# Kernel tuning notes

Measured on AMD Instinct MI355X. Metric: run time of the kernel, lower is better.

The kernel has to match this reference:

```python
import jax, jax.numpy as jnp
import numpy as np

THRESHOLD = 0.5
EPS = 1e-6

def cxcywh_to_xyxy(b):
    return jnp.concatenate([b[..., :2] - b[..., 2:] / 2, b[..., :2] + b[..., 2:] / 2], axis=-1)

def xyxy_to_cxcywh(b):
    return jnp.concatenate([(b[..., :2] + b[..., 2:]) / 2, b[..., 2:] - b[..., :2]], axis=-1)

def iou_matrix(a, b, eps):
    # a: [P,4] xyxy, b: [O,4] xyxy -> [P,O]
    lb = jnp.maximum(a[:, None, :2], b[None, :, :2])
    ub = jnp.minimum(a[:, None, 2:], b[None, :, 2:])
    wh = jnp.clip(ub - lb, 0.0)
    inter = wh[..., 0] * wh[..., 1]
    area_a = (a[:, 2] - a[:, 0]) * (a[:, 3] - a[:, 1])
    area_b = (b[:, 2] - b[:, 0]) * (b[:, 3] - b[:, 1])
    union = area_a[:, None] + area_b[None, :] - inter
    return inter / (union + eps)

def match_single(priors_xyxy, t_xyxy, t_labels):
    # SSD-style matching (stand-in for Calculate_bbox_target_classes)
    n_obj = t_xyxy.shape[0]
    iou = iou_matrix(priors_xyxy, t_xyxy, EPS)          # [P,O]
    best_obj_iou = jnp.max(iou, axis=1)                 # [P]
    best_obj = jnp.argmax(iou, axis=1)                  # [P]
    best_prior = jnp.argmax(iou, axis=0)                # [O] force-match each object
    best_obj = best_obj.at[best_prior].set(jnp.arange(n_obj))
    best_obj_iou = best_obj_iou.at[best_prior].set(1.0)
    labels = t_labels[best_obj]                          # [P]
    labels = jnp.where(best_obj_iou < THRESHOLD, 0, labels)
    locs = xyxy_to_cxcywh(t_xyxy[best_obj])              # [P,4] cxcywh
    return labels, locs

def setup_inputs() -> dict:
    key = jax.random.key(0)
    k1, k2, k3, k4, k5, k6, k7 = jax.random.split(key, 7)
    B, P, C, O = 64, 8732, 81, 32
    # predictions: cxcywh-ish boxes in [0,1]
    pl_xy = jax.random.uniform(k1, (B, P, 2))
    pl_wh = jax.random.uniform(k2, (B, P, 2)) * 0.25 + 0.02
    predictlocs = jnp.concatenate([pl_xy, pl_wh], axis=-1)
    predictcls = jax.random.normal(k3, (B, P, C))
    pr_xy = jax.random.uniform(k4, (P, 2))
    pr_wh = jax.random.uniform(k5, (P, 2)) * 0.25 + 0.02
    prior_bboxes = jnp.concatenate([pr_xy, pr_wh], axis=-1)
    tb_xy = jax.random.uniform(k6, (B, O, 2)) * 0.8
    tb_wh = jax.random.uniform(k7, (B, O, 2)) * 0.2 + 0.02
    target_bboxes = jnp.concatenate([tb_xy, tb_wh], axis=-1)  # xywh
    target_labels = jax.random.randint(jax.random.fold_in(key, 99), (B, O), 1, C)
    return {"predictlocs": predictlocs, "predictcls": predictcls,
            "prior_bboxes": prior_bboxes, "target_bboxes": target_bboxes,
            "target_labels": target_labels}

def _iou_loss_masked(pred_cxcywh, tgt_cxcywh, pos_mask):
    tp = cxcywh_to_xyxy(tgt_cxcywh)
    bp = cxcywh_to_xyxy(pred_cxcywh)
    lb = jnp.maximum(tp[..., :2], bp[..., :2])
    ub = jnp.minimum(tp[..., 2:], bp[..., 2:])
    wh = jnp.clip(ub - lb, 0.0)
    inter = wh[..., 0] * wh[..., 1]
    area_b = (bp[..., 2] - bp[..., 0]) * (bp[..., 3] - bp[..., 1])
    area_t = (tp[..., 2] - tp[..., 0]) * (tp[..., 3] - tp[..., 1])
    union = area_t + area_b - inter
    v = 1.0 - inter / (union + EPS)
    n_pos = jnp.sum(pos_mask)
    return jnp.sum(jnp.where(pos_mask, v, 0.0)) / n_pos

def reference(predictlocs, predictcls, prior_bboxes, target_bboxes, target_labels):
    n_classes = predictcls.shape[2]
    # xywh -> xyxy, as in original forward
    t_xyxy = jnp.concatenate([target_bboxes[..., :2],
                              target_bboxes[..., :2] + target_bboxes[..., 2:]], axis=-1)
    priors_xyxy = cxcywh_to_xyxy(prior_bboxes)
    true_classes, true_locs = jax.vmap(match_single, in_axes=(None, 0, 0))(
        priors_xyxy, t_xyxy, target_labels)      # [B,P], [B,P,4]
    pos = true_classes != 0                       # [B,P]
    n_pos = jnp.sum(pos).astype(predictlocs.dtype)
    # IoU loss over positives (mean over positives)
    iou_loss = _iou_loss_masked(predictlocs, true_locs, pos)
    # L1 loss (mean over all elements of selected [Npos,4])
    l1 = jnp.abs(predictlocs - true_locs)
    loc_loss = jnp.sum(jnp.where(pos[..., None], l1, 0.0)) / (n_pos * 4.0)
    # CrossEntropy over all priors (mean)
    logp = jax.nn.log_softmax(predictcls.reshape(-1, n_classes), axis=-1)
    cross_loss = -jnp.mean(jnp.take_along_axis(
        logp, true_classes.reshape(-1, 1), axis=-1))
    return loc_loss, cross_loss, iou_loss
```

## Files before the change

kernel.cpp:

```cpp
#include <hip/hip_runtime.h>
#include <hip/hip_bf16.h>

#define NB 64
#define NP 8732
#define NO 32
#define NC 81
#define NROWS (NB * NP)
#define PBLK 2183


__device__ __forceinline__ float ldT(const float* p, size_t i) { return p[i]; }
__device__ __forceinline__ float ldT(const unsigned short* p, size_t i) {
    return __uint_as_float((unsigned)p[i] << 16);
}
__device__ __forceinline__ float4 ld4(const float* p, size_t i) {
    return *(const float4*)(p + i);
}
__device__ __forceinline__ float4 ld4(const unsigned short* p, size_t i) {
    ushort4 u = *(const ushort4*)(p + i);
    return make_float4(__uint_as_float((unsigned)u.x << 16),
                       __uint_as_float((unsigned)u.y << 16),
                       __uint_as_float((unsigned)u.z << 16),
                       __uint_as_float((unsigned)u.w << 16));
}

template <int CTRL>
__device__ __forceinline__ float dppf(float x) {
    return __int_as_float(__builtin_amdgcn_update_dpp(
        0, __float_as_int(x), CTRL, 0xF, 0xF, true));
}
#define DPP_RED16(var, OP)                      \
    var = OP(var, dppf<0x128>(var));            \
    var = OP(var, dppf<0x124>(var));            \
    var = OP(var, dppf<0x122>(var));            \
    var = OP(var, dppf<0x121>(var));
__device__ __forceinline__ float addf(float a, float b) { return a + b; }

__global__ void init_kernel(const void* __restrict__ prior,
                            unsigned long long* __restrict__ bestPrior,
                            float* __restrict__ accum, int* __restrict__ flag) {
    int i = threadIdx.x;
    for (int j = i; j < NB * NO; j += blockDim.x) bestPrior[j] = 0ull;
    if (i < 4) accum[i] = 0.0f;
    if (i < 64) {
        const unsigned short* pb = (const unsigned short*)prior;
        float v = __uint_as_float((unsigned)pb[i] << 16);
        unsigned long long bad = __ballot(!(fabsf(v) <= 8.0f));
        if (i == 0) *flag = (__popcll(bad) >= 8) ? 1 : 0;
    }
}

template <typename T>
__device__ __forceinline__ void match_body(
        const T* __restrict__ prior, const T* __restrict__ tb,
        unsigned long long* __restrict__ bestPrior) {
    const int b   = blockIdx.y;
    const int o   = threadIdx.x & 31;
    const int seg = threadIdx.x >> 5;
    const int p0  = blockIdx.x * 256 + seg * 32;

    float4 t = ld4(tb, ((size_t)(b * NO + o)) * 4);
    float tx0 = t.x, ty0 = t.y, tx1 = t.x + t.z, ty1 = t.y + t.w, ta = t.z * t.w;

    float bi = -1.0f;
    int bp = 0;
    for (int j = 0; j < 32; ++j) {
        int p = p0 + j;
        if (p >= NP) break;
        float4 pr = ld4(prior, (size_t)p * 4);
        float px0 = pr.x - pr.z * 0.5f, py0 = pr.y - pr.w * 0.5f;
        float px1 = pr.x + pr.z * 0.5f, py1 = pr.y + pr.w * 0.5f;
        float pa = (px1 - px0) * (py1 - py0);
        float lbx = fmaxf(px0, tx0), lby = fmaxf(py0, ty0);
        float ubx = fminf(px1, tx1), uby = fminf(py1, ty1);
        float ww = fmaxf(ubx - lbx, 0.0f), hh = fmaxf(uby - lby, 0.0f);
        float inter = ww * hh;
        float iou = inter / (pa + ta - inter + 1e-6f);
        if (iou > bi) { bi = iou; bp = p; }
    }
    if (bi >= 0.0f) {
        unsigned long long packed =
            (((unsigned long long)__float_as_uint(bi)) << 32) | (~(unsigned)bp);
        atomicMax(&bestPrior[b * NO + o], packed);
    }
}

__global__ __launch_bounds__(256) void match_kernel(
        const void* __restrict__ prior, const void* __restrict__ tb,
        unsigned long long* __restrict__ bestPrior, const int* __restrict__ flag) {
    if (*flag)
        match_body<float>((const float*)prior, (const float*)tb, bestPrior);
    else
        match_body<unsigned short>((const unsigned short*)prior,
                                   (const unsigned short*)tb, bestPrior);
}

template <typename T>
__device__ __forceinline__ void ce_load(
        const T* __restrict__ pcls, const unsigned char* s_lab8,
        int i, int g, int q, int rbase,
        float (&v)[4][5], float (&v80)[4], float (&xl)[4]) {
    #pragma unroll
    for (int s = 0; s < 4; ++s) {
        int rl = i * 16 + g + s * 64;
        int labv = s_lab8[rl];
        const T* xr = pcls + (size_t)(rbase + rl) * NC;
        #pragma unroll
        for (int j = 0; j < 5; ++j) v[s][j] = ldT(xr, q + 16 * j);
        v80[s] = -1e30f; xl[s] = 0.f;
        if (q == 0) {
            v80[s] = ldT(xr, 80);
            xl[s] = ldT(xr, labv);
        }
    }
}

__device__ __forceinline__ void ce_compute(
        const float (&v)[4][5], const float (&v80)[4], const float (&xl)[4],
        int q, float& c_sum) {
    #pragma unroll
    for (int s = 0; s < 4; ++s) {
        float mm = fmaxf(fmaxf(fmaxf(v[s][0], v[s][1]), fmaxf(v[s][2], v[s][3])),
                         fmaxf(v[s][4], v80[s]));
        DPP_RED16(mm, fmaxf)
        float ss = __expf(v[s][0] - mm) + __expf(v[s][1] - mm)
                 + __expf(v[s][2] - mm) + __expf(v[s][3] - mm)
                 + __expf(v[s][4] - mm) + __expf(v80[s] - mm);
        DPP_RED16(ss, addf)
        if (q == 0) c_sum += (mm + __logf(ss)) - xl[s];
    }
}

template <typename T>
__device__ void prepce_impl(
        const T* __restrict__ plocs, const T* __restrict__ prior,
        const T* __restrict__ tb, const int* __restrict__ tlab,
        const unsigned long long* __restrict__ bestPrior,
        const T* __restrict__ pcls, float* __restrict__ accum) {
    __shared__ float4 s_box[2][NO];
    __shared__ float  s_area[2][NO];
    __shared__ int    s_lab[2][NO];
    __shared__ unsigned s_forced[2][NO];
    __shared__ unsigned char s_lab8[256];
    __shared__ float red[4][4];

    const int tid = threadIdx.x;
    const int lane = tid & 63;
    const int wv = tid >> 6;
    const int row = blockIdx.x * 256 + tid;
    const int b = row / NP;
    const int p = row - b * NP;
    const int b0 = (blockIdx.x * 256) / NP;

    if (tid < 64) {
        int bb = tid >> 5, o = tid & 31;
        int bq = b0 + bb;
        if (bq < NB) {
            float4 t = ld4(tb, ((size_t)(bq * NO + o)) * 4);
            s_box[bb][o] = make_float4(t.x, t.y, t.x + t.z, t.y + t.w);
            s_area[bb][o] = t.z * t.w;
            s_lab[bb][o] = tlab[bq * NO + o];
            s_forced[bb][o] = ~(unsigned)(bestPrior[bq * NO + o] & 0xffffffffull);
        }
    }
    __syncthreads();

    const int bb = b - b0;
    float4 pr = ld4(prior, (size_t)p * 4);
    float px0 = pr.x - pr.z * 0.5f, py0 = pr.y - pr.w * 0.5f;
    float px1 = pr.x + pr.z * 0.5f, py1 = pr.y + pr.w * 0.5f;
    float pa = (px1 - px0) * (py1 - py0);

    float bi = -1.0f;
    int bo = 0, fo = -1;
    #pragma unroll 8
    for (int o = 0; o < NO; ++o) {
        float4 t = s_box[bb][o];
        float lbx = fmaxf(px0, t.x), lby = fmaxf(py0, t.y);
        float ubx = fminf(px1, t.z), uby = fminf(py1, t.w);
        float ww = fmaxf(ubx - lbx, 0.0f), hh = fmaxf(uby - lby, 0.0f);
        float inter = ww * hh;
        float iou = inter / (pa + s_area[bb][o] - inter + 1e-6f);
        if (iou > bi) { bi = iou; bo = o; }
        if (s_forced[bb][o] == (unsigned)p) fo = o;
    }
    if (fo >= 0) { bo = fo; bi = 1.0f; }

    int lab = s_lab[bb][bo];
    if (bi < 0.5f) lab = 0;
    s_lab8[tid] = (unsigned char)lab;

    float l1_sum = 0.f, iou_sum = 0.f, np_sum = 0.f;
    if (lab != 0) {
        np_sum = 1.0f;
        float4 t = s_box[bb][bo];
        float x0 = t.x, y0 = t.y, x1 = t.z, y1 = t.w;
        float4 traw = ld4(tb, ((size_t)(b * NO + bo)) * 4);
        float tcx = (x0 + x1) * 0.5f, tcy = (y0 + y1) * 0.5f;
        float4 qv = ld4(plocs, (size_t)row * 4);
        l1_sum = fabsf(qv.x - tcx) + fabsf(qv.y - tcy)
               + fabsf(qv.z - traw.z) + fabsf(qv.w - traw.w);
        float qX0 = qv.x - qv.z * 0.5f, qY0 = qv.y - qv.w * 0.5f;
        float qX1 = qv.x + qv.z * 0.5f, qY1 = qv.y + qv.w * 0.5f;
        float lbx = fmaxf(x0, qX0), lby = fmaxf(y0, qY0);
        float ubx = fminf(x1, qX1), uby = fminf(y1, qY1);
        float iw = fmaxf(ubx - lbx, 0.f), ih = fmaxf(uby - lby, 0.f);
        float inter = iw * ih;
        float areaq = (qX1 - qX0) * (qY1 - qY0);
        float areat = (x1 - x0) * (y1 - y0);
        iou_sum = 1.0f - inter / (areat + areaq - inter + 1e-6f);
    }

    __syncthreads();

    const int q = lane & 15;
    const int g = wv * 4 + (lane >> 4);
    const int rbase = blockIdx.x * 256;
    float c_sum = 0.f;

    float vA[4][5], vB[4][5];
    float v80A[4], v80B[4], xlA[4], xlB[4];

    ce_load(pcls, s_lab8, 0, g, q, rbase, vA, v80A, xlA);
    ce_load(pcls, s_lab8, 1, g, q, rbase, vB, v80B, xlB);
    __builtin_amdgcn_sched_barrier(0);
    ce_compute(vA, v80A, xlA, q, c_sum);
    ce_load(pcls, s_lab8, 2, g, q, rbase, vA, v80A, xlA);
    __builtin_amdgcn_sched_barrier(0);
    ce_compute(vB, v80B, xlB, q, c_sum);
    ce_load(pcls, s_lab8, 3, g, q, rbase, vB, v80B, xlB);
    __builtin_amdgcn_sched_barrier(0);
    ce_compute(vA, v80A, xlA, q, c_sum);
    ce_compute(vB, v80B, xlB, q, c_sum);

    #pragma unroll
    for (int d = 1; d < 64; d <<= 1) {
        c_sum   += __shfl_xor(c_sum, d);
        l1_sum  += __shfl_xor(l1_sum, d);
        iou_sum += __shfl_xor(iou_sum, d);
        np_sum  += __shfl_xor(np_sum, d);
    }
    if (lane == 0) {
        red[wv][0] = c_sum; red[wv][1] = l1_sum;
        red[wv][2] = iou_sum; red[wv][3] = np_sum;
    }
    __syncthreads();
    if (tid == 0) {
        float a0 = 0, a1 = 0, a2 = 0, a3 = 0;
        for (int k = 0; k < 4; ++k) {
            a0 += red[k][0]; a1 += red[k][1]; a2 += red[k][2]; a3 += red[k][3];
        }
        atomicAdd(&accum[0], a0);
        atomicAdd(&accum[1], a1);
        atomicAdd(&accum[2], a2);
        atomicAdd(&accum[3], a3);
    }
}

__global__ __launch_bounds__(256) void prepce_kernel(
        const void* __restrict__ plocs, const void* __restrict__ prior,
        const void* __restrict__ tb, const int* __restrict__ tlab,
        const unsigned long long* __restrict__ bestPrior,
        const void* __restrict__ pcls,
        const int* __restrict__ flag, float* __restrict__ accum) {
    if (*flag)
        prepce_impl<float>((const float*)plocs, (const float*)prior,
                           (const float*)tb, tlab, bestPrior,
                           (const float*)pcls, accum);
    else
        prepce_impl<unsigned short>((const unsigned short*)plocs,
                                    (const unsigned short*)prior,
                                    (const unsigned short*)tb,
                                    tlab, bestPrior,
                                    (const unsigned short*)pcls, accum);
}

__global__ void finalize_kernel(const float* __restrict__ accum,
                                const int* __restrict__ flag, void* __restrict__ out) {
    if (threadIdx.x == 0) {
        float cross = accum[0] / (float)NROWS;
        float npos = accum[3];
        float loc = accum[1] / (npos * 4.0f);
        float iou = accum[2] / npos;
        if (*flag) {
            float* o = (float*)out;
            o[0] = loc; o[1] = cross; o[2] = iou;
        } else {
            __hip_bfloat16* o = (__hip_bfloat16*)out;
            o[0] = __float2bfloat16(loc);
            o[1] = __float2bfloat16(cross);
            o[2] = __float2bfloat16(iou);
        }
    }
}

extern "C" void kernel_launch(void* const* d_in, const int* in_sizes, int n_in,
                              void* d_out, int out_size, void* d_ws, size_t ws_size,
                              hipStream_t stream) {
    const void* plocs = d_in[0];
    const void* pcls  = d_in[1];
    const void* prior = d_in[2];
    const void* tb    = d_in[3];
    const int*  tlab  = (const int*)d_in[4];

    char* w = (char*)d_ws;
    unsigned long long* bestPrior = (unsigned long long*)w;
    float* accum = (float*)(w + 16384);
    int*   flag  = (int*)(w + 16400);

    hipLaunchKernelGGL(init_kernel, dim3(1), dim3(256), 0, stream,
                       prior, bestPrior, accum, flag);

    dim3 gA((NP + 255) / 256, NB);
    hipLaunchKernelGGL(match_kernel, gA, dim3(256), 0, stream,
                       prior, tb, bestPrior, flag);

    hipLaunchKernelGGL(prepce_kernel, dim3(PBLK), dim3(256), 0, stream,
                       plocs, prior, tb, tlab, bestPrior, pcls, flag, accum);

    hipLaunchKernelGGL(finalize_kernel, dim3(1), dim3(64), 0, stream,
                       accum, flag, d_out);
}
```

Before: 363.4 us.

## Stage class logits through LDS with async global_load_lds double buffering

Replaces the direct per-lane global loads of the cross-entropy logits with async global-to-LDS copies of 64-row tiles, double-buffered across four quarters. The first tile is issued before the IoU matching work so the load can overlap it. The intent is fully coalesced 16-byte loads instead of strided scalar row reads. In exchange it adds about 41KB of LDS per block, which lowers occupancy, and a block-wide barrier after each quarter.

```diff
diff --git a/kernel.cpp b/kernel.cpp
--- a/kernel.cpp
+++ b/kernel.cpp
@@ -22,6 +22,12 @@
                        __uint_as_float((unsigned)u.y << 16),
                        __uint_as_float((unsigned)u.z << 16),
                        __uint_as_float((unsigned)u.w << 16));
+}
+
+__device__ __forceinline__ void g2lds16(const void* g, void* l) {
+    __builtin_amdgcn_global_load_lds(
+        (const __attribute__((address_space(1))) void*)g,
+        (__attribute__((address_space(3))) void*)l, 16, 0, 0);
 }
 
 template <int CTRL>
@@ -96,38 +102,29 @@
 }
 
 template <typename T>
-__device__ __forceinline__ void ce_load(
-        const T* __restrict__ pcls, const unsigned char* s_lab8,
-        int i, int g, int q, int rbase,
-        float (&v)[4][5], float (&v80)[4], float (&xl)[4]) {
+__device__ __forceinline__ void ce_quarter(
+        const T* tile, const unsigned char* s_lab8, int qoff,
+        int g, int q, float& c_sum) {
     #pragma unroll
-    for (int s = 0; s < 4; ++s) {
-        int rl = i * 16 + g + s * 64;
-        int labv = s_lab8[rl];
-        const T* xr = pcls + (size_t)(rbase + rl) * NC;
-        #pragma unroll
-        for (int j = 0; j < 5; ++j) v[s][j] = ldT(xr, q + 16 * j);
-        v80[s] = -1e30f; xl[s] = 0.f;
-        if (q == 0) {
-            v80[s] = ldT(xr, 80);
-            xl[s] = ldT(xr, labv);
-        }
-    }
-}
-
-__device__ __forceinline__ void ce_compute(
-        const float (&v)[4][5], const float (&v80)[4], const float (&xl)[4],
-        int q, float& c_sum) {
-    #pragma unroll
-    for (int s = 0; s < 4; ++s) {
-        float mm = fmaxf(fmaxf(fmaxf(v[s][0], v[s][1]), fmaxf(v[s][2], v[s][3])),
-                         fmaxf(v[s][4], v80[s]));
+    for (int i = 0; i < 4; ++i) {
+        int rl = i * 16 + g;
+        int labv = s_lab8[qoff + rl];
+        const T* xr = tile + rl * NC;
+        float v0 = ldT(xr, q);
+        float v1 = ldT(xr, q + 16);
+        float v2 = ldT(xr, q + 32);
+        float v3 = ldT(xr, q + 48);
+        float v4 = ldT(xr, q + 64);
+        float v80 = ldT(xr, 80);
+        float xlv = ldT(xr, labv);
+        float e80 = (q == 0) ? v80 : -1e30f;
+        float mm = fmaxf(fmaxf(fmaxf(v0, v1), fmaxf(v2, v3)), fmaxf(v4, e80));
         DPP_RED16(mm, fmaxf)
-        float ss = __expf(v[s][0] - mm) + __expf(v[s][1] - mm)
-                 + __expf(v[s][2] - mm) + __expf(v[s][3] - mm)
-                 + __expf(v[s][4] - mm) + __expf(v80[s] - mm);
+        float ss = __expf(v0 - mm) + __expf(v1 - mm) + __expf(v2 - mm)
+                 + __expf(v3 - mm) + __expf(v4 - mm) + __expf(e80 - mm);
         DPP_RED16(ss, addf)
-        if (q == 0) c_sum += (mm + __logf(ss)) - xl[s];
+        float term = (mm + __logf(ss)) - xlv;
+        c_sum += (q == 0) ? term : 0.0f;
     }
 }
 
@@ -143,14 +140,16 @@
     __shared__ unsigned s_forced[2][NO];
     __shared__ unsigned char s_lab8[256];
     __shared__ float red[4][4];
+    __shared__ alignas(16) char s_tile[2][64 * NC * 4];
 
     const int tid = threadIdx.x;
     const int lane = tid & 63;
     const int wv = tid >> 6;
-    const int row = blockIdx.x * 256 + tid;
+    const int rbase = blockIdx.x * 256;
+    const int row = rbase + tid;
     const int b = row / NP;
     const int p = row - b * NP;
-    const int b0 = (blockIdx.x * 256) / NP;
+    const int b0 = rbase / NP;
 
     if (tid < 64) {
         int bb = tid >> 5, o = tid & 31;
@@ -164,6 +163,22 @@
         }
     }
     __syncthreads();
+
+    constexpr int QBYTES = 64 * NC * (int)sizeof(T);
+    constexpr int N16 = QBYTES / 16;
+    constexpr int KMAX = (N16 + 255) / 256;
+    const char* gbase = (const char*)(pcls + (size_t)rbase * NC);
+    auto stage = [&](int buf, int qq) {
+        const char* gq = gbase + (size_t)qq * QBYTES;
+        #pragma unroll
+        for (int k = 0; k < KMAX; ++k) {
+            int base16 = k * 256 + wv * 64;
+            int idx = base16 + lane;
+            if (idx < N16)
+                g2lds16(gq + (size_t)idx * 16, s_tile[buf] + base16 * 16);
+        }
+    };
+    stage(0, 0);
 
     const int bb = b - b0;
     float4 pr = ld4(prior, (size_t)p * 4);
@@ -211,27 +226,29 @@
         iou_sum = 1.0f - inter / (areat + areaq - inter + 1e-6f);
     }
 
+    asm volatile("s_waitcnt vmcnt(0)" ::: "memory");
     __syncthreads();
 
     const int q = lane & 15;
     const int g = wv * 4 + (lane >> 4);
-    const int rbase = blockIdx.x * 256;
     float c_sum = 0.f;
 
-    float vA[4][5], vB[4][5];
-    float v80A[4], v80B[4], xlA[4], xlB[4];
-
-    ce_load(pcls, s_lab8, 0, g, q, rbase, vA, v80A, xlA);
-    ce_load(pcls, s_lab8, 1, g, q, rbase, vB, v80B, xlB);
-    __builtin_amdgcn_sched_barrier(0);
-    ce_compute(vA, v80A, xlA, q, c_sum);
-    ce_load(pcls, s_lab8, 2, g, q, rbase, vA, v80A, xlA);
-    __builtin_amdgcn_sched_barrier(0);
-    ce_compute(vB, v80B, xlB, q, c_sum);
-    ce_load(pcls, s_lab8, 3, g, q, rbase, vB, v80B, xlB);
-    __builtin_amdgcn_sched_barrier(0);
-    ce_compute(vA, v80A, xlA, q, c_sum);
-    ce_compute(vB, v80B, xlB, q, c_sum);
+    stage(1, 1);
+    ce_quarter((const T*)s_tile[0], s_lab8, 0, g, q, c_sum);
+    asm volatile("s_waitcnt vmcnt(0)" ::: "memory");
+    __syncthreads();
+
+    stage(0, 2);
+    ce_quarter((const T*)s_tile[1], s_lab8, 64, g, q, c_sum);
+    asm volatile("s_waitcnt vmcnt(0)" ::: "memory");
+    __syncthreads();
+
+    stage(1, 3);
+    ce_quarter((const T*)s_tile[0], s_lab8, 128, g, q, c_sum);
+    asm volatile("s_waitcnt vmcnt(0)" ::: "memory");
+    __syncthreads();
+
+    ce_quarter((const T*)s_tile[1], s_lab8, 192, g, q, c_sum);
 
     #pragma unroll
     for (int d = 1; d < 64; d <<= 1) {
```

Result: no change. 367.9 us (+1.2%).
